# Performance work log

Measured on AMD Instinct MI355X. Metric: run time of the kernel, lower is better.

The kernel has to match this reference:

```python
import jax, jax.numpy as jnp
import numpy as np

IN_DIM = 512
OUT_DIM = 512


def _fo_pool(z, f):
    # z, f: [T, B, H]; c_t = f_t * c_{t-1} + (1 - f_t) * z_t, c_0 = 0
    # Linear recurrence -> parallel associative scan over time axis.
    a = f
    b = (1.0 - f) * z

    def combine(x1, x2):
        a1, b1 = x1
        a2, b2 = x2
        return a2 * a1, a2 * b1 + b2

    _, c = jax.lax.associative_scan(combine, (a, b), axis=0)
    return c


def _qrnn(x, W, b):
    # x: [T, B, D] -> h: [T, B, H]. Eval mode (zoneout dropout disabled).
    g = jnp.einsum('tbd,dh->tbh', x, W) + b          # [T, B, 3H]
    z, f, o = jnp.split(g, 3, axis=-1)
    z = jnp.tanh(z)
    f = jax.nn.sigmoid(f)
    o = jax.nn.sigmoid(o)
    c = _fo_pool(z, f)
    return o * c


def setup_inputs() -> dict:
    key = jax.random.key(0)
    k = jax.random.split(key, 5)
    B, T = 32, 2048
    s = 1.0 / np.sqrt(IN_DIM)
    x = jax.random.normal(k[0], (B, T, IN_DIM), dtype=jnp.float32)
    W_f = jax.random.uniform(k[1], (IN_DIM, 3 * OUT_DIM), jnp.float32, -s, s)
    b_f = jax.random.uniform(k[2], (3 * OUT_DIM,), jnp.float32, -s, s)
    W_b = jax.random.uniform(k[3], (IN_DIM, 3 * OUT_DIM), jnp.float32, -s, s)
    b_b = jax.random.uniform(k[4], (3 * OUT_DIM,), jnp.float32, -s, s)
    return {"x": x, "W_f": W_f, "b_f": b_f, "W_b": W_b, "b_b": b_b}


def reference(x, W_f, b_f, W_b, b_b):
    xt = jnp.transpose(x, (1, 0, 2))                 # [T, B, D]
    h_f = _qrnn(xt, W_f, b_f)
    # Source bug reproduced: ts = list(range(T)) does NOT reverse the sequence,
    # so the 'backward' QRNN sees the same (unreversed) input.
    h_b = _qrnn(xt, W_b, b_b)
    h = jnp.concatenate((h_f, h_b), axis=-1)         # [T, B, 2H]
    return jnp.transpose(h, (1, 0, 2))               # return_sequences=True
```

## Files before the change

kernel.cpp:

```cpp
#include <hip/hip_runtime.h>
#include <hip/hip_fp16.h>

typedef __attribute__((ext_vector_type(8))) short short8;
typedef __attribute__((ext_vector_type(4))) float f32x4;

#define TT 2048
#define DD 512

__device__ __forceinline__ unsigned short f2bf(float f) {
  unsigned int u = __float_as_uint(f);
  u += 0x7FFFu + ((u >> 16) & 1u);
  return (unsigned short)(u >> 16);
}
__device__ __forceinline__ float h2f(unsigned short u) {
  return __half2float(__ushort_as_half(u));
}
__device__ __forceinline__ unsigned int pkrtz(float a, float b) {
  auto r = __builtin_amdgcn_cvt_pkrtz(a, b);
  return __builtin_bit_cast(unsigned int, r);
}
__device__ __forceinline__ void gload16(const void* g, void* l) {
  __builtin_amdgcn_global_load_lds((const __attribute__((address_space(1))) void*)g,
                                   (__attribute__((address_space(3))) void*)l, 16, 0, 0);
}


__global__ void xconv_kernel(const float* __restrict__ x, unsigned short* __restrict__ xbf) {
  int i = blockIdx.x * 256 + threadIdx.x;
  const float4* p = (const float4*)x + (size_t)i * 2;
  float4 a = p[0], b = p[1];
  short8 o;
  o[0] = f2bf(a.x); o[1] = f2bf(a.y); o[2] = f2bf(a.z); o[3] = f2bf(a.w);
  o[4] = f2bf(b.x); o[5] = f2bf(b.y); o[6] = f2bf(b.z); o[7] = f2bf(b.w);
  *((short8*)xbf + i) = o;
}

__global__ void wtrans_new_kernel(const float* __restrict__ Wf,
                                  const float* __restrict__ Wb,
                                  unsigned short* __restrict__ wt) {
  __shared__ float tile[32][33];
  int bid = blockIdx.x;
  int d   = bid / 768;
  int rem = bid - d * 768;
  int kt = rem & 15;
  int ct = rem >> 4;
  const float* W = d ? Wb : Wf;
  int k0 = kt * 32, c0 = ct * 32;
  int r = threadIdx.x >> 5, c = threadIdx.x & 31;
#pragma unroll
  for (int i = 0; i < 4; i++)
    tile[r + 8*i][c] = W[(size_t)(k0 + r + 8*i) * 1536 + c0 + c];
  __syncthreads();
#pragma unroll
  for (int i = 0; i < 4; i++) {
    int col = c0 + r + 8*i;
    int gate = col >> 9, hh = col & 511;
    int nn = (hh >> 6) * 192 + gate * 64 + (hh & 63);
    wt[((size_t)d * 1536 + nn) * 512 + k0 + c] = f2bf(tile[c][r + 8*i]);
  }
}

__global__ void wtrans_old_kernel(const float* __restrict__ Wf,
                                  const float* __restrict__ Wb,
                                  unsigned short* __restrict__ wt) {
  __shared__ float tile[32][33];
  int bid = blockIdx.x;
  int d   = bid / 768;
  int rem = bid - d * 768;
  int kt = rem & 15;
  int ct = rem >> 4;
  const float* W = d ? Wb : Wf;
  int k0 = kt * 32, c0 = ct * 32;
  int r = threadIdx.x >> 5, c = threadIdx.x & 31;
#pragma unroll
  for (int i = 0; i < 4; i++)
    tile[r + 8*i][c] = W[(size_t)(k0 + r + 8*i) * 1536 + c0 + c];
  __syncthreads();
  unsigned short* outp = wt + ((size_t)d * 1536 + c0) * 512 + k0;
#pragma unroll
  for (int i = 0; i < 4; i++)
    outp[(size_t)(r + 8*i) * 512 + c] = f2bf(tile[c][r + 8*i]);
}

__global__ void cbias_kernel(const float* __restrict__ bf_, const float* __restrict__ bb_,
                             float* __restrict__ cb) {
  int t = blockIdx.x * 256 + threadIdx.x;
  int d = t / 1536, cc = t - d * 1536;
  int gate = cc >> 9, hh = cc & 511;
  int nn = (hh >> 6) * 192 + gate * 64 + (hh & 63);
  cb[d * 1536 + nn] = (d ? bb_ : bf_)[cc];
}

__global__ __launch_bounds__(256, 2)
void qrnn_persist_kernel(const unsigned short* __restrict__ xbf,
                         const unsigned short* __restrict__ wtp,
                         const float* __restrict__ cb,
                         float* __restrict__ out) {
  __shared__ __align__(16) char smem[51712];

  int bid = blockIdx.x;
  int bid2 = (bid & 7) * 64 + (bid >> 3);
  int b = bid2 >> 4;
  int v = bid2 & 15;
  int dir = v >> 3, hb = v & 7;
  int nbase = dir * 1536 + hb * 192;
  int obase = dir * 512 + hb * 64;

  int tid = threadIdx.x, lane = tid & 63, wv = tid >> 6;

  int aoff[2];
#pragma unroll
  for (int mf = 0; mf < 2; ++mf) {
    int row = wv * 32 + mf * 16 + (lane & 15);
    aoff[mf] = row * 128 + (((lane >> 4) * 16) ^ ((row & 7) << 4));
  }
  int boff[12];
#pragma unroll
  for (int j = 0; j < 12; ++j) {
    int row = j * 16 + (lane & 15);
    boff[j] = 16384 + row * 128 + (((lane >> 4) * 16) ^ ((row & 7) << 4));
  }

  float cbv[12];
#pragma unroll
  for (int j = 0; j < 12; ++j)
    cbv[j] = cb[nbase + j * 16 + (lane & 15)];

  const char* bS[6];
#pragma unroll
  for (int i = 0; i < 6; ++i) {
    int l = tid + 256 * i, row = l >> 3;
    int koff = ((l & 7) * 16) ^ ((row & 7) << 4);
    bS[i] = (const char*)wtp + (size_t)(nbase + row) * 1024 + koff;
  }
  int a_row[4], a_koff[4];
#pragma unroll
  for (int i = 0; i < 4; ++i) {
    int l = tid + 256 * i;
    a_row[i] = l >> 3;
    a_koff[i] = ((l & 7) * 16) ^ ((a_row[i] & 7) << 4);
  }

  int h = tid & 63, sub = tid >> 6;
  const char* zB = smem + h * 256;
  const char* fB = smem + 16384 + h * 256;
  const char* oB = smem + 32768 + h * 256;
  int sx = h << 2;
  float2* abL = (float2*)(smem + 49152);

  float c_chunk = 0.f;

  for (int ck = 0; ck < 16; ++ck) {
    size_t m0 = (size_t)b * TT + ck * 128;
    const char* aBase = (const char*)xbf + m0 * 1024;

    f32x4 acc[2][12];
#pragma unroll
    for (int mf = 0; mf < 2; ++mf)
#pragma unroll
      for (int j = 0; j < 12; ++j)
        acc[mf][j] = f32x4{0.f, 0.f, 0.f, 0.f};

    for (int kt = 0; kt < 8; ++kt) {
      __syncthreads();
      int kb = kt * 128;
#pragma unroll
      for (int i = 0; i < 4; ++i)
        gload16(aBase + (size_t)a_row[i] * 1024 + a_koff[i] + kb, smem + tid * 16 + i * 4096);
#pragma unroll
      for (int i = 0; i < 6; ++i)
        gload16(bS[i] + kb, smem + 16384 + tid * 16 + i * 4096);
      __syncthreads();
#pragma unroll
      for (int ks = 0; ks < 2; ++ks) {
        int kx = ks * 64;
        short8 a0 = *(const short8*)(smem + (aoff[0] ^ kx));
        short8 a1 = *(const short8*)(smem + (aoff[1] ^ kx));
#pragma unroll
        for (int g = 0; g < 3; ++g) {
          short8 b0 = *(const short8*)(smem + (boff[4*g+0] ^ kx));
          short8 b1 = *(const short8*)(smem + (boff[4*g+1] ^ kx));
          short8 b2 = *(const short8*)(smem + (boff[4*g+2] ^ kx));
          short8 b3 = *(const short8*)(smem + (boff[4*g+3] ^ kx));
          acc[0][4*g+0] = __builtin_amdgcn_mfma_f32_16x16x32_bf16(a0, b0, acc[0][4*g+0], 0, 0, 0);
          acc[1][4*g+0] = __builtin_amdgcn_mfma_f32_16x16x32_bf16(a1, b0, acc[1][4*g+0], 0, 0, 0);
          acc[0][4*g+1] = __builtin_amdgcn_mfma_f32_16x16x32_bf16(a0, b1, acc[0][4*g+1], 0, 0, 0);
          acc[1][4*g+1] = __builtin_amdgcn_mfma_f32_16x16x32_bf16(a1, b1, acc[1][4*g+1], 0, 0, 0);
          acc[0][4*g+2] = __builtin_amdgcn_mfma_f32_16x16x32_bf16(a0, b2, acc[0][4*g+2], 0, 0, 0);
          acc[1][4*g+2] = __builtin_amdgcn_mfma_f32_16x16x32_bf16(a1, b2, acc[1][4*g+2], 0, 0, 0);
          acc[0][4*g+3] = __builtin_amdgcn_mfma_f32_16x16x32_bf16(a0, b3, acc[0][4*g+3], 0, 0, 0);
          acc[1][4*g+3] = __builtin_amdgcn_mfma_f32_16x16x32_bf16(a1, b3, acc[1][4*g+3], 0, 0, 0);
        }
      }
    }

    __syncthreads();

#pragma unroll
    for (int mf = 0; mf < 2; ++mf) {
      int base_t = wv * 32 + mf * 16 + (lane >> 4) * 4;
#pragma unroll
      for (int j = 0; j < 12; ++j) {
        int g = j >> 2;
        int hsub = (j & 3) * 16 + (lane & 15);
        float vv[4], a[4];
#pragma unroll
        for (int r = 0; r < 4; ++r) vv[r] = acc[mf][j][r] + cbv[j];
        if (g == 0) {
#pragma unroll
          for (int r = 0; r < 4; ++r) {
            float e = __expf(2.f * vv[r]);
            a[r] = 1.f - 2.f * __builtin_amdgcn_rcpf(e + 1.f);
          }
        } else {
#pragma unroll
          for (int r = 0; r < 4; ++r)
            a[r] = __builtin_amdgcn_rcpf(1.f + __expf(-vv[r]));
        }
        char* gp = smem + g * 16384 + hsub * 256;
        int sw = hsub << 2;
        *(unsigned int*)(gp + ((2 * base_t) ^ sw))     = pkrtz(a[0], a[1]);
        *(unsigned int*)(gp + ((2 * base_t + 4) ^ sw)) = pkrtz(a[2], a[3]);
      }
    }

    __syncthreads();

    unsigned int zw[16], fw[16];
    float A = 1.f, Bv = 0.f;
#pragma unroll
    for (int i = 0; i < 16; ++i) {
      int byo = (sub * 64 + 4 * i) ^ sx;
      zw[i] = *(const unsigned int*)(zB + byo);
      fw[i] = *(const unsigned int*)(fB + byo);
      float z0 = h2f((unsigned short)zw[i]), z1 = h2f((unsigned short)(zw[i] >> 16));
      float f0 = h2f((unsigned short)fw[i]), f1 = h2f((unsigned short)(fw[i] >> 16));
      Bv = f0 * Bv + (1.f - f0) * z0;
      Bv = f1 * Bv + (1.f - f1) * z1;
      A *= f0 * f1;
    }
    abL[h * 5 + sub] = float2{A, Bv};

    __syncthreads();

    float cs = c_chunk, cn = c_chunk;
#pragma unroll
    for (int s = 0; s < 4; ++s) {
      float2 ab = abL[h * 5 + s];
      if (s == sub) cs = cn;
      cn = ab.x * cn + ab.y;
    }
    c_chunk = cn;

    float c = cs;
    float* op = out + (m0 + sub * 32) * 1024 + obase + h;
#pragma unroll
    for (int i = 0; i < 16; ++i) {
      int byo = (sub * 64 + 4 * i) ^ sx;
      unsigned int oo = *(const unsigned int*)(oB + byo);
      float z0 = h2f((unsigned short)zw[i]), z1 = h2f((unsigned short)(zw[i] >> 16));
      float f0 = h2f((unsigned short)fw[i]), f1 = h2f((unsigned short)(fw[i] >> 16));
      float o0 = h2f((unsigned short)oo), o1 = h2f((unsigned short)(oo >> 16));
      c = f0 * c + (1.f - f0) * z0;
      op[0] = o0 * c;
      c = f1 * c + (1.f - f1) * z1;
      op[1024] = o1 * c;
      op += 2048;
    }
  }
}

#define NB 192
#define BT 64
__global__ __launch_bounds__(256, 2)
void qrnn_kernel(const float* __restrict__ x,
                 const float* __restrict__ bf_, const float* __restrict__ bb_,
                 const unsigned short* __restrict__ wt,
                 float* __restrict__ out) {
  __shared__ __align__(16) unsigned short sA[64 * 64];
  __shared__ float sG[64 * 193];
  __shared__ float sBias[NB];
  const int tid  = threadIdx.x;
  const int lane = tid & 63;
  const int wv   = tid >> 6;
  int p = blockIdx.x;
  int xcd = p & 7, slot = p >> 3;
  int b   = xcd * 4 + (slot >> 4);
  int v   = slot & 15;
  int dir = v >> 3, ht = v & 7;
  int h0  = ht * 64;
  if (tid < NB) {
    const float* bsrc = dir ? bb_ : bf_;
    sBias[tid] = bsrc[((tid >> 6) << 9) + h0 + (tid & 63)];
  }
  const float* xb = x + (size_t)b * TT * DD;
  const unsigned short* wtd = wt + (size_t)dir * 1536 * 512;
  size_t brow[3];
#pragma unroll
  for (int j = 0; j < 3; j++) {
    int n = 48 * wv + 16 * j + (lane & 15);
    brow[j] = (size_t)(((n >> 6) << 9) + h0 + (n & 63)) * 512 + 8 * (lane >> 4);
  }
  int a_off[2][4];
#pragma unroll
  for (int kk = 0; kk < 2; kk++)
#pragma unroll
    for (int m = 0; m < 4; m++) {
      int row = 16 * m + (lane & 15);
      a_off[kk][m] = row * 128 + ((64 * kk + 16 * (lane >> 4)) ^ ((row & 7) << 4));
    }
  int s_trow[4], s_kq[4], s_woff[4];
#pragma unroll
  for (int i = 0; i < 4; i++) {
    int q = tid + 256 * i;
    s_trow[i] = q >> 4;
    s_kq[i]   = q & 15;
    s_woff[i] = s_trow[i] * 128 + ((8 * s_kq[i]) ^ ((s_trow[i] & 7) << 4));
  }
  float c = 0.f;
  f32x4 acc[4][3];
  for (int t0 = 0; t0 < TT; t0 += BT) {
#pragma unroll
    for (int m = 0; m < 4; m++)
#pragma unroll
      for (int j = 0; j < 3; j++)
        acc[m][j] = f32x4{0.f, 0.f, 0.f, 0.f};
    float4 vv[4];
#pragma unroll
    for (int i = 0; i < 4; i++)
      vv[i] = *(const float4*)(xb + (size_t)(t0 + s_trow[i]) * DD + 4 * s_kq[i]);
#pragma unroll
    for (int ks = 0; ks < 8; ks++) {
      __syncthreads();
#pragma unroll
      for (int i = 0; i < 4; i++) {
        ushort4 u;
        u.x = f2bf(vv[i].x); u.y = f2bf(vv[i].y);
        u.z = f2bf(vv[i].z); u.w = f2bf(vv[i].w);
        *(ushort4*)((char*)sA + s_woff[i]) = u;
      }
      if (ks < 7) {
        int k0n = (ks + 1) * 64;
#pragma unroll
        for (int i = 0; i < 4; i++)
          vv[i] = *(const float4*)(xb + (size_t)(t0 + s_trow[i]) * DD + k0n + 4 * s_kq[i]);
      }
      __syncthreads();
      const char* sAb = (const char*)sA;
      int k0 = ks * 64;
#pragma unroll
      for (int kk = 0; kk < 2; kk++) {
        short8 bfr[3];
#pragma unroll
        for (int j = 0; j < 3; j++)
          bfr[j] = *(const short8*)(wtd + brow[j] + k0 + 32 * kk);
#pragma unroll
        for (int m = 0; m < 4; m++) {
          short8 afr = *(const short8*)(sAb + a_off[kk][m]);
#pragma unroll
          for (int j = 0; j < 3; j++)
            acc[m][j] = __builtin_amdgcn_mfma_f32_16x16x32_bf16(afr, bfr[j], acc[m][j], 0, 0, 0);
        }
      }
    }
#pragma unroll
    for (int m = 0; m < 4; m++)
#pragma unroll
      for (int j = 0; j < 3; j++) {
        int col   = 48 * wv + 16 * j + (lane & 15);
        int rbase = 16 * m + 4 * (lane >> 4);
#pragma unroll
        for (int r = 0; r < 4; r++)
          sG[(rbase + r) * 193 + col] = acc[m][j][r];
      }
    __syncthreads();
    for (int idx = tid; idx < 64 * NB; idx += 256) {
      int t = idx / NB;
      int n = idx - t * NB;
      float g = sG[t * 193 + n] + sBias[n];
      float res;
      if (n < 64) { float e = __expf(2.f * g); res = 1.f - 2.f / (e + 1.f); }
      else        { res = 1.f / (1.f + __expf(-g)); }
      sG[t * 193 + n] = res;
    }
    __syncthreads();
    if (tid < 64) {
      float* og = out + ((size_t)(b * TT + t0)) * 1024 + (dir << 9) + h0 + tid;
      float cc = c;
#pragma unroll 8
      for (int t = 0; t < BT; t++) {
        float z = sG[t * 193 + tid];
        float f = sG[t * 193 + 64 + tid];
        float o = sG[t * 193 + 128 + tid];
        cc = z + f * (cc - z);
        og[(size_t)t << 10] = o * cc;
      }
      c = cc;
    }
  }
}

extern "C" void kernel_launch(void* const* d_in, const int* in_sizes, int n_in,
                              void* d_out, int out_size, void* d_ws, size_t ws_size,
                              hipStream_t stream) {
  const float* x   = (const float*)d_in[0];
  const float* W_f = (const float*)d_in[1];
  const float* b_f = (const float*)d_in[2];
  const float* W_b = (const float*)d_in[3];
  const float* b_b = (const float*)d_in[4];
  float* out = (float*)d_out;

  char* ws = (char*)d_ws;
  const size_t OFF_WT  = 0;
  const size_t OFF_CB  = 3145728;
  const size_t OFF_XBF = 3158016;
  const size_t NEED    = OFF_XBF + 67108864ull;

  unsigned short* wt  = (unsigned short*)(ws + OFF_WT);
  float* cbias        = (float*)(ws + OFF_CB);
  unsigned short* xbf = (unsigned short*)(ws + OFF_XBF);

  if (ws_size >= NEED) {
    xconv_kernel<<<16384, 256, 0, stream>>>(x, xbf);
    wtrans_new_kernel<<<1536, 256, 0, stream>>>(W_f, W_b, wt);
    cbias_kernel<<<12, 256, 0, stream>>>(b_f, b_b, cbias);
    qrnn_persist_kernel<<<512, 256, 0, stream>>>(xbf, wt, cbias, out);
  } else {
    wtrans_old_kernel<<<1536, 256, 0, stream>>>(W_f, W_b, wt);
    qrnn_kernel<<<512, 256, 0, stream>>>(x, b_f, b_b, wt, out);
  }
}
```

Baseline: 307.6 us.

## Double-buffer LDS tiles to overlap global loads with MFMA compute

Splits the GEMM staging area into two LDS buffers so the next K-tile is fetched by global-to-LDS loads while MFMAs run on the current one. The two block-wide syncs per K step become one wait plus one barrier, and the K loop is fully unrolled. LDS per block grows from about 51 KB to 80 KB, which may cut the two-blocks-per-CU occupancy and risks a race if the epilogue region that reuses smem overlaps the buffers being loaded.

```diff
diff --git a/kernel.cpp b/kernel.cpp
--- a/kernel.cpp
+++ b/kernel.cpp
@@ -96,7 +96,7 @@
                          const unsigned short* __restrict__ wtp,
                          const float* __restrict__ cb,
                          float* __restrict__ out) {
-  __shared__ __align__(16) char smem[51712];
+  __shared__ __align__(16) char smem[81920];
 
   int bid = blockIdx.x;
   int bid2 = (bid & 7) * 64 + (bid >> 3);
@@ -154,6 +154,19 @@
     size_t m0 = (size_t)b * TT + ck * 128;
     const char* aBase = (const char*)xbf + m0 * 1024;
 
+#define STAGE(KT)                                                              \
+    {                                                                          \
+      int kb_ = (KT) * 128;                                                    \
+      char* dst_ = smem + ((KT) & 1) * 40960;                                  \
+      _Pragma("unroll")                                                        \
+      for (int i = 0; i < 4; ++i)                                              \
+        gload16(aBase + (size_t)a_row[i] * 1024 + a_koff[i] + kb_,             \
+                dst_ + tid * 16 + i * 4096);                                   \
+      _Pragma("unroll")                                                        \
+      for (int i = 0; i < 6; ++i)                                              \
+        gload16(bS[i] + kb_, dst_ + 16384 + tid * 16 + i * 4096);              \
+    }
+
     f32x4 acc[2][12];
 #pragma unroll
     for (int mf = 0; mf < 2; ++mf)
@@ -161,27 +174,26 @@
       for (int j = 0; j < 12; ++j)
         acc[mf][j] = f32x4{0.f, 0.f, 0.f, 0.f};
 
+    __builtin_amdgcn_s_barrier();
+    STAGE(0)
+    asm volatile("s_waitcnt vmcnt(0)" ::: "memory");
+    __builtin_amdgcn_s_barrier();
+
+#pragma unroll
     for (int kt = 0; kt < 8; ++kt) {
-      __syncthreads();
-      int kb = kt * 128;
-#pragma unroll
-      for (int i = 0; i < 4; ++i)
-        gload16(aBase + (size_t)a_row[i] * 1024 + a_koff[i] + kb, smem + tid * 16 + i * 4096);
-#pragma unroll
-      for (int i = 0; i < 6; ++i)
-        gload16(bS[i] + kb, smem + 16384 + tid * 16 + i * 4096);
-      __syncthreads();
+      if (kt < 7) STAGE(kt + 1)
+      const char* base = smem + (kt & 1) * 40960;
 #pragma unroll
       for (int ks = 0; ks < 2; ++ks) {
         int kx = ks * 64;
-        short8 a0 = *(const short8*)(smem + (aoff[0] ^ kx));
-        short8 a1 = *(const short8*)(smem + (aoff[1] ^ kx));
+        short8 a0 = *(const short8*)(base + (aoff[0] ^ kx));
+        short8 a1 = *(const short8*)(base + (aoff[1] ^ kx));
 #pragma unroll
         for (int g = 0; g < 3; ++g) {
-          short8 b0 = *(const short8*)(smem + (boff[4*g+0] ^ kx));
-          short8 b1 = *(const short8*)(smem + (boff[4*g+1] ^ kx));
-          short8 b2 = *(const short8*)(smem + (boff[4*g+2] ^ kx));
-          short8 b3 = *(const short8*)(smem + (boff[4*g+3] ^ kx));
+          short8 b0 = *(const short8*)(base + (boff[4*g+0] ^ kx));
+          short8 b1 = *(const short8*)(base + (boff[4*g+1] ^ kx));
+          short8 b2 = *(const short8*)(base + (boff[4*g+2] ^ kx));
+          short8 b3 = *(const short8*)(base + (boff[4*g+3] ^ kx));
           acc[0][4*g+0] = __builtin_amdgcn_mfma_f32_16x16x32_bf16(a0, b0, acc[0][4*g+0], 0, 0, 0);
           acc[1][4*g+0] = __builtin_amdgcn_mfma_f32_16x16x32_bf16(a1, b0, acc[1][4*g+0], 0, 0, 0);
           acc[0][4*g+1] = __builtin_amdgcn_mfma_f32_16x16x32_bf16(a0, b1, acc[0][4*g+1], 0, 0, 0);
@@ -192,9 +204,14 @@
           acc[1][4*g+3] = __builtin_amdgcn_mfma_f32_16x16x32_bf16(a1, b3, acc[1][4*g+3], 0, 0, 0);
         }
       }
-    }
-
-    __syncthreads();
+      if (kt < 7) {
+        asm volatile("s_waitcnt vmcnt(0)" ::: "memory");
+        __builtin_amdgcn_s_barrier();
+      }
+    }
+#undef STAGE
+
+    __builtin_amdgcn_s_barrier();
 
 #pragma unroll
     for (int mf = 0; mf < 2; ++mf) {
```

New measurement: 478.4 us. +55.5%, slower.

## Retile GEMM waves into a 2x2 grid and raise MFMA priority

Applied to the files above, without the earlier changes.

Changes the per-wave tile from 32 rows by all 192 columns to a 2x2 wave grid of 64 rows by 96 columns. This cuts LDS fragment reads per MFMA (10 loads for 24 MFMAs instead of 14). All fragment loads are hoisted ahead of the MFMA burst, and the burst is wrapped in s_setprio. __syncthreads is replaced by a raw s_barrier, which drops the implicit waitcnt and risks the LDS DMA data not yet being visible when the MFMAs read it. The epilogue gate index now comes from the column, so g can vary within a wave's column tile. That adds divergence in the tanh/sigmoid branch.

```diff
diff --git a/kernel.cpp b/kernel.cpp
--- a/kernel.cpp
+++ b/kernel.cpp
@@ -107,24 +107,25 @@
   int obase = dir * 512 + hb * 64;
 
   int tid = threadIdx.x, lane = tid & 63, wv = tid >> 6;
-
-  int aoff[2];
-#pragma unroll
-  for (int mf = 0; mf < 2; ++mf) {
-    int row = wv * 32 + mf * 16 + (lane & 15);
+  int wr = wv >> 1, wc = wv & 1;
+
+  int aoff[4];
+#pragma unroll
+  for (int mf = 0; mf < 4; ++mf) {
+    int row = wr * 64 + mf * 16 + (lane & 15);
     aoff[mf] = row * 128 + (((lane >> 4) * 16) ^ ((row & 7) << 4));
   }
-  int boff[12];
-#pragma unroll
-  for (int j = 0; j < 12; ++j) {
-    int row = j * 16 + (lane & 15);
+  int boff[6];
+#pragma unroll
+  for (int j = 0; j < 6; ++j) {
+    int row = wc * 96 + j * 16 + (lane & 15);
     boff[j] = 16384 + row * 128 + (((lane >> 4) * 16) ^ ((row & 7) << 4));
   }
 
-  float cbv[12];
-#pragma unroll
-  for (int j = 0; j < 12; ++j)
-    cbv[j] = cb[nbase + j * 16 + (lane & 15)];
+  float cbv[6];
+#pragma unroll
+  for (int j = 0; j < 6; ++j)
+    cbv[j] = cb[nbase + wc * 96 + j * 16 + (lane & 15)];
 
   const char* bS[6];
 #pragma unroll
@@ -154,15 +155,15 @@
     size_t m0 = (size_t)b * TT + ck * 128;
     const char* aBase = (const char*)xbf + m0 * 1024;
 
-    f32x4 acc[2][12];
-#pragma unroll
-    for (int mf = 0; mf < 2; ++mf)
-#pragma unroll
-      for (int j = 0; j < 12; ++j)
+    f32x4 acc[4][6];
+#pragma unroll
+    for (int mf = 0; mf < 4; ++mf)
+#pragma unroll
+      for (int j = 0; j < 6; ++j)
         acc[mf][j] = f32x4{0.f, 0.f, 0.f, 0.f};
 
     for (int kt = 0; kt < 8; ++kt) {
-      __syncthreads();
+      __builtin_amdgcn_s_barrier();
       int kb = kt * 128;
 #pragma unroll
       for (int i = 0; i < 4; ++i)
@@ -174,35 +175,33 @@
 #pragma unroll
       for (int ks = 0; ks < 2; ++ks) {
         int kx = ks * 64;
-        short8 a0 = *(const short8*)(smem + (aoff[0] ^ kx));
-        short8 a1 = *(const short8*)(smem + (aoff[1] ^ kx));
-#pragma unroll
-        for (int g = 0; g < 3; ++g) {
-          short8 b0 = *(const short8*)(smem + (boff[4*g+0] ^ kx));
-          short8 b1 = *(const short8*)(smem + (boff[4*g+1] ^ kx));
-          short8 b2 = *(const short8*)(smem + (boff[4*g+2] ^ kx));
-          short8 b3 = *(const short8*)(smem + (boff[4*g+3] ^ kx));
-          acc[0][4*g+0] = __builtin_amdgcn_mfma_f32_16x16x32_bf16(a0, b0, acc[0][4*g+0], 0, 0, 0);
-          acc[1][4*g+0] = __builtin_amdgcn_mfma_f32_16x16x32_bf16(a1, b0, acc[1][4*g+0], 0, 0, 0);
-          acc[0][4*g+1] = __builtin_amdgcn_mfma_f32_16x16x32_bf16(a0, b1, acc[0][4*g+1], 0, 0, 0);
-          acc[1][4*g+1] = __builtin_amdgcn_mfma_f32_16x16x32_bf16(a1, b1, acc[1][4*g+1], 0, 0, 0);
-          acc[0][4*g+2] = __builtin_amdgcn_mfma_f32_16x16x32_bf16(a0, b2, acc[0][4*g+2], 0, 0, 0);
-          acc[1][4*g+2] = __builtin_amdgcn_mfma_f32_16x16x32_bf16(a1, b2, acc[1][4*g+2], 0, 0, 0);
-          acc[0][4*g+3] = __builtin_amdgcn_mfma_f32_16x16x32_bf16(a0, b3, acc[0][4*g+3], 0, 0, 0);
-          acc[1][4*g+3] = __builtin_amdgcn_mfma_f32_16x16x32_bf16(a1, b3, acc[1][4*g+3], 0, 0, 0);
-        }
-      }
-    }
-
-    __syncthreads();
-
-#pragma unroll
-    for (int mf = 0; mf < 2; ++mf) {
-      int base_t = wv * 32 + mf * 16 + (lane >> 4) * 4;
-#pragma unroll
-      for (int j = 0; j < 12; ++j) {
-        int g = j >> 2;
-        int hsub = (j & 3) * 16 + (lane & 15);
+        short8 av[4], bv[6];
+#pragma unroll
+        for (int mf = 0; mf < 4; ++mf)
+          av[mf] = *(const short8*)(smem + (aoff[mf] ^ kx));
+#pragma unroll
+        for (int j = 0; j < 6; ++j)
+          bv[j] = *(const short8*)(smem + (boff[j] ^ kx));
+        __builtin_amdgcn_s_setprio(1);
+#pragma unroll
+        for (int mf = 0; mf < 4; ++mf)
+#pragma unroll
+          for (int j = 0; j < 6; ++j)
+            acc[mf][j] = __builtin_amdgcn_mfma_f32_16x16x32_bf16(av[mf], bv[j], acc[mf][j], 0, 0, 0);
+        __builtin_amdgcn_s_setprio(0);
+      }
+    }
+
+    __builtin_amdgcn_s_barrier();
+
+#pragma unroll
+    for (int mf = 0; mf < 4; ++mf) {
+      int base_t = wr * 64 + mf * 16 + (lane >> 4) * 4;
+#pragma unroll
+      for (int j = 0; j < 6; ++j) {
+        int nn = wc * 96 + j * 16 + (lane & 15);
+        int g = nn >> 6;
+        int hsub = nn & 63;
         float vv[4], a[4];
 #pragma unroll
         for (int r = 0; r < 4; ++r) vv[r] = acc[mf][j][r] + cbv[j];
```

Result: slower. 315.4 us (+2.5%).

## Compute QRNN scan directly from MFMA accumulators instead of staging gates in LDS

Applied to the files above, without the earlier changes.

The epilogue no longer packs the activated z/f/o gates to fp16 in shared memory and rereads them per hidden unit. Each lane now runs a local scan over its 4 accumulator rows, combines partial (A,B) pairs across lanes and then across waves through a small LDS buffer, and writes outputs straight from registers. This removes the fp16 gate staging, one barrier and most LDS traffic, and keeps gates in fp32. The cost is higher register pressure and output stores strided by 1024 floats per row (each lane writes 4 rows), which may coalesce worse than before.

```diff
diff --git a/kernel.cpp b/kernel.cpp
--- a/kernel.cpp
+++ b/kernel.cpp
@@ -11,13 +11,6 @@
   unsigned int u = __float_as_uint(f);
   u += 0x7FFFu + ((u >> 16) & 1u);
   return (unsigned short)(u >> 16);
-}
-__device__ __forceinline__ float h2f(unsigned short u) {
-  return __half2float(__ushort_as_half(u));
-}
-__device__ __forceinline__ unsigned int pkrtz(float a, float b) {
-  auto r = __builtin_amdgcn_cvt_pkrtz(a, b);
-  return __builtin_bit_cast(unsigned int, r);
 }
 __device__ __forceinline__ void gload16(const void* g, void* l) {
   __builtin_amdgcn_global_load_lds((const __attribute__((address_space(1))) void*)g,
@@ -96,7 +89,7 @@
                          const unsigned short* __restrict__ wtp,
                          const float* __restrict__ cb,
                          float* __restrict__ out) {
-  __shared__ __align__(16) char smem[51712];
+  __shared__ __align__(16) char smem[40960];
 
   int bid = blockIdx.x;
   int bid2 = (bid & 7) * 64 + (bid >> 3);
@@ -107,24 +100,25 @@
   int obase = dir * 512 + hb * 64;
 
   int tid = threadIdx.x, lane = tid & 63, wv = tid >> 6;
+  int l15 = lane & 15, q = lane >> 4;
 
   int aoff[2];
 #pragma unroll
   for (int mf = 0; mf < 2; ++mf) {
-    int row = wv * 32 + mf * 16 + (lane & 15);
-    aoff[mf] = row * 128 + (((lane >> 4) * 16) ^ ((row & 7) << 4));
+    int row = wv * 32 + mf * 16 + l15;
+    aoff[mf] = row * 128 + ((q * 16) ^ ((row & 7) << 4));
   }
   int boff[12];
 #pragma unroll
   for (int j = 0; j < 12; ++j) {
-    int row = j * 16 + (lane & 15);
-    boff[j] = 16384 + row * 128 + (((lane >> 4) * 16) ^ ((row & 7) << 4));
+    int row = j * 16 + l15;
+    boff[j] = 16384 + row * 128 + ((q * 16) ^ ((row & 7) << 4));
   }
 
   float cbv[12];
 #pragma unroll
   for (int j = 0; j < 12; ++j)
-    cbv[j] = cb[nbase + j * 16 + (lane & 15)];
+    cbv[j] = cb[nbase + j * 16 + l15];
 
   const char* bS[6];
 #pragma unroll
@@ -141,14 +135,10 @@
     a_koff[i] = ((l & 7) * 16) ^ ((a_row[i] & 7) << 4);
   }
 
-  int h = tid & 63, sub = tid >> 6;
-  const char* zB = smem + h * 256;
-  const char* fB = smem + 16384 + h * 256;
-  const char* oB = smem + 32768 + h * 256;
-  int sx = h << 2;
-  float2* abL = (float2*)(smem + 49152);
-
-  float c_chunk = 0.f;
+  float2* abR = (float2*)smem;
+  float2* abL = (float2*)(smem + 18432);
+
+  float c_chunk[4] = {0.f, 0.f, 0.f, 0.f};
 
   for (int ck = 0; ck < 16; ++ck) {
     size_t m0 = (size_t)b * TT + ck * 128;
@@ -194,78 +184,85 @@
       }
     }
 
+    __builtin_amdgcn_s_barrier();
+
+#pragma unroll
+    for (int mf = 0; mf < 2; ++mf)
+#pragma unroll
+      for (int j = 0; j < 12; ++j)
+#pragma unroll
+        for (int r = 0; r < 4; ++r) {
+          float g = acc[mf][j][r] + cbv[j];
+          if (j < 4) {
+            float e = __expf(2.f * g);
+            acc[mf][j][r] = 1.f - 2.f * __builtin_amdgcn_rcpf(e + 1.f);
+          } else {
+            acc[mf][j][r] = __builtin_amdgcn_rcpf(1.f + __expf(-g));
+          }
+        }
+
+#pragma unroll
+    for (int jj = 0; jj < 4; ++jj) {
+      int hj = 16 * jj + l15;
+#pragma unroll
+      for (int mf = 0; mf < 2; ++mf) {
+        float A = 1.f, Bv = 0.f;
+#pragma unroll
+        for (int r = 0; r < 4; ++r) {
+          float f = acc[mf][4 + jj][r], z = acc[mf][jj][r];
+          Bv = f * Bv + (1.f - f) * z;
+          A *= f;
+        }
+        abR[(wv * 64 + hj) * 9 + mf * 4 + q] = float2{A, Bv};
+      }
+    }
+
+    float sAx[2][4], sBx[2][4];
+#pragma unroll
+    for (int jj = 0; jj < 4; ++jj) {
+      int hj = 16 * jj + l15;
+      float Ar = 1.f, Br = 0.f;
+#pragma unroll
+      for (int s = 0; s < 8; ++s) {
+        if (s == q)     { sAx[0][jj] = Ar; sBx[0][jj] = Br; }
+        if (s == 4 + q) { sAx[1][jj] = Ar; sBx[1][jj] = Br; }
+        float2 ab = abR[(wv * 64 + hj) * 9 + s];
+        Ar = ab.x * Ar;
+        Br = ab.x * Br + ab.y;
+      }
+      if (q == 0) abL[wv * 64 + hj] = float2{Ar, Br};
+    }
+
     __syncthreads();
 
+    float wentry[4];
+#pragma unroll
+    for (int jj = 0; jj < 4; ++jj) {
+      int hj = 16 * jj + l15;
+      float cc = c_chunk[jj];
+#pragma unroll
+      for (int w = 0; w < 4; ++w) {
+        if (w == wv) wentry[jj] = cc;
+        float2 t = abL[w * 64 + hj];
+        cc = t.x * cc + t.y;
+      }
+      c_chunk[jj] = cc;
+    }
+
 #pragma unroll
     for (int mf = 0; mf < 2; ++mf) {
-      int base_t = wv * 32 + mf * 16 + (lane >> 4) * 4;
-#pragma unroll
-      for (int j = 0; j < 12; ++j) {
-        int g = j >> 2;
-        int hsub = (j & 3) * 16 + (lane & 15);
-        float vv[4], a[4];
-#pragma unroll
-        for (int r = 0; r < 4; ++r) vv[r] = acc[mf][j][r] + cbv[j];
-        if (g == 0) {
-#pragma unroll
-          for (int r = 0; r < 4; ++r) {
-            float e = __expf(2.f * vv[r]);
-            a[r] = 1.f - 2.f * __builtin_amdgcn_rcpf(e + 1.f);
-          }
-        } else {
-#pragma unroll
-          for (int r = 0; r < 4; ++r)
-            a[r] = __builtin_amdgcn_rcpf(1.f + __expf(-vv[r]));
+      int t0 = wv * 32 + mf * 16 + 4 * q;
+#pragma unroll
+      for (int jj = 0; jj < 4; ++jj) {
+        float c = sAx[mf][jj] * wentry[jj] + sBx[mf][jj];
+        float* op = out + (m0 + t0) * 1024 + obase + 16 * jj + l15;
+#pragma unroll
+        for (int r = 0; r < 4; ++r) {
+          float f = acc[mf][4 + jj][r], z = acc[mf][jj][r], o = acc[mf][8 + jj][r];
+          c = f * c + (1.f - f) * z;
+          op[(size_t)r * 1024] = o * c;
         }
-        char* gp = smem + g * 16384 + hsub * 256;
-        int sw = hsub << 2;
-        *(unsigned int*)(gp + ((2 * base_t) ^ sw))     = pkrtz(a[0], a[1]);
-        *(unsigned int*)(gp + ((2 * base_t + 4) ^ sw)) = pkrtz(a[2], a[3]);
-      }
-    }
-
-    __syncthreads();
-
-    unsigned int zw[16], fw[16];
-    float A = 1.f, Bv = 0.f;
-#pragma unroll
-    for (int i = 0; i < 16; ++i) {
-      int byo = (sub * 64 + 4 * i) ^ sx;
-      zw[i] = *(const unsigned int*)(zB + byo);
-      fw[i] = *(const unsigned int*)(fB + byo);
-      float z0 = h2f((unsigned short)zw[i]), z1 = h2f((unsigned short)(zw[i] >> 16));
-      float f0 = h2f((unsigned short)fw[i]), f1 = h2f((unsigned short)(fw[i] >> 16));
-      Bv = f0 * Bv + (1.f - f0) * z0;
-      Bv = f1 * Bv + (1.f - f1) * z1;
-      A *= f0 * f1;
-    }
-    abL[h * 5 + sub] = float2{A, Bv};
-
-    __syncthreads();
-
-    float cs = c_chunk, cn = c_chunk;
-#pragma unroll
-    for (int s = 0; s < 4; ++s) {
-      float2 ab = abL[h * 5 + s];
-      if (s == sub) cs = cn;
-      cn = ab.x * cn + ab.y;
-    }
-    c_chunk = cn;
-
-    float c = cs;
-    float* op = out + (m0 + sub * 32) * 1024 + obase + h;
-#pragma unroll
-    for (int i = 0; i < 16; ++i) {
-      int byo = (sub * 64 + 4 * i) ^ sx;
-      unsigned int oo = *(const unsigned int*)(oB + byo);
-      float z0 = h2f((unsigned short)zw[i]), z1 = h2f((unsigned short)(zw[i] >> 16));
-      float f0 = h2f((unsigned short)fw[i]), f1 = h2f((unsigned short)(fw[i] >> 16));
-      float o0 = h2f((unsigned short)oo), o1 = h2f((unsigned short)(oo >> 16));
-      c = f0 * c + (1.f - f0) * z0;
-      op[0] = o0 * c;
-      c = f1 * c + (1.f - f1) * z1;
-      op[1024] = o1 * c;
-      op += 2048;
+      }
     }
   }
 }
```

Measured after the change: 426.4 us. 1.39x slower.
